# Optimization experiments

Hardware: AMD Instinct MI355X
Metric: run time of the kernel (lower is better)

The kernel has to match this reference:

```python
import jax, jax.numpy as jnp
import numpy as np

L, H, DM, DH, DI = 6, 8, 512, 64, 2048
QLEN, BSZ, MLEN = 256, 32, 256
EPS = 1e-5


def _ln(x, g, b):
    mu = jnp.mean(x, axis=-1, keepdims=True)
    var = jnp.var(x, axis=-1, keepdims=True)
    return (x - mu) * jax.lax.rsqrt(var + EPS) * g + b


def _rel_shift(x):
    # x: [qlen, rlen, bsz, n_head] -> Transformer-XL relative shift
    q, r, b, n = x.shape
    zp = jnp.zeros((q, 1, b, n), x.dtype)
    xp = jnp.concatenate([zp, x], axis=1).reshape(r + 1, q, b, n)
    return xp[1:].reshape(q, r, b, n)


def setup_inputs() -> dict:
    key = jax.random.key(0)
    ks = jax.random.split(key, 12)
    s = 0.02
    return {
        "w": jax.random.normal(ks[0], (QLEN, BSZ, DM), jnp.float32),
        "mems": jax.random.normal(ks[1], (L, MLEN, BSZ, DM), jnp.float32),
        "qkv_w": jax.random.normal(ks[2], (L, DM, 3 * H * DH), jnp.float32) * s,
        "r_net_w": jax.random.normal(ks[3], (L, DM, H * DH), jnp.float32) * s,
        "o_w": jax.random.normal(ks[4], (L, H * DH, DM), jnp.float32) * s,
        "ln1_g": jnp.ones((L, DM), jnp.float32),
        "ln1_b": jnp.zeros((L, DM), jnp.float32),
        "ff_w1": jax.random.normal(ks[5], (L, DM, DI), jnp.float32) * s,
        "ff_b1": jnp.zeros((L, DI), jnp.float32),
        "ff_w2": jax.random.normal(ks[6], (L, DI, DM), jnp.float32) * s,
        "ff_b2": jnp.zeros((L, DM), jnp.float32),
        "ln2_g": jnp.ones((L, DM), jnp.float32),
        "ln2_b": jnp.zeros((L, DM), jnp.float32),
        "r_w_bias": jax.random.normal(ks[7], (H, DH), jnp.float32) * s,
        "r_r_bias": jax.random.normal(ks[8], (H, DH), jnp.float32) * s,
    }


def reference(w, mems, qkv_w, r_net_w, o_w, ln1_g, ln1_b,
              ff_w1, ff_b1, ff_w2, ff_b2, ln2_g, ln2_b,
              r_w_bias, r_r_bias):
    qlen, bsz, d_model = w.shape
    mlen = mems.shape[1]
    klen = qlen + mlen
    scale = 1.0 / (DH ** 0.5)

    # sinusoidal relative positional embedding, pos = klen-1 ... 0
    pos_seq = jnp.arange(klen - 1, -1, -1, dtype=jnp.float32)
    inv_freq = 1.0 / (10000.0 ** (jnp.arange(0, d_model, 2, dtype=jnp.float32) / d_model))
    sinu = pos_seq[:, None] * inv_freq[None, :]
    r = jnp.concatenate([jnp.sin(sinu), jnp.cos(sinu)], axis=-1)  # [klen, d_model]

    # causal mask with memory: query i attends keys j <= i + mlen
    mask = jnp.triu(jnp.ones((qlen, klen), bool), k=1 + mlen)

    h = w
    for l in range(L):
        cat = jnp.concatenate([mems[l], h], axis=0)            # [klen, b, d]
        w_heads = cat @ qkv_w[l]                                # [klen, b, 3HD]
        q, k, v = jnp.split(w_heads, 3, axis=-1)
        q = q[-qlen:].reshape(qlen, bsz, H, DH)
        k = k.reshape(klen, bsz, H, DH)
        v = v.reshape(klen, bsz, H, DH)
        r_head_k = (r @ r_net_w[l]).reshape(klen, H, DH)

        AC = jnp.einsum('ibnd,jbnd->ijbn', q + r_w_bias, k)
        BD = _rel_shift(jnp.einsum('ibnd,jnd->ijbn', q + r_r_bias, r_head_k))
        score = (AC + BD) * scale
        score = jnp.where(mask[:, :, None, None], -jnp.inf, score)
        prob = jax.nn.softmax(score, axis=1)                    # over key dim j
        vec = jnp.einsum('ijbn,jbnd->ibnd', prob, v).reshape(qlen, bsz, H * DH)
        attn_out = vec @ o_w[l]
        h = _ln(h + attn_out, ln1_g[l], ln1_b[l])

        ff = jax.nn.relu(h @ ff_w1[l] + ff_b1[l]) @ ff_w2[l] + ff_b2[l]
        h = _ln(h + ff, ln2_g[l], ln2_b[l])
    return h
```

## Files before the change

kernel.cpp:

```cpp
#include <hip/hip_runtime.h>
#include <math.h>

#define LNUM 6
#define H 8
#define DM 512
#define DH 64
#define DI 2048
#define QLEN 256
#define BSZ 32
#define MLEN 256
#define KLEN (QLEN + MLEN)
#define EPS 1e-5f
#define SCALE 0.125f
#define SN 1024

typedef unsigned short u16;
typedef short bf16x8 __attribute__((ext_vector_type(8)));
typedef short bf16x4 __attribute__((ext_vector_type(4)));
typedef float f32x4 __attribute__((ext_vector_type(4)));

__device__ __forceinline__ u16 f2b(float f) {
    union { float f; unsigned u; } x; x.f = f;
    const unsigned r = x.u + 0x7FFFu + ((x.u >> 16) & 1u);
    return (u16)(r >> 16);
}
__device__ __forceinline__ float b2f(u16 b) {
    union { unsigned u; float f; } x; x.u = (unsigned)b << 16;
    return x.f;
}

__device__ __forceinline__ void gl16(const u16* g, u16* l) {
    __builtin_amdgcn_global_load_lds(
        (const __attribute__((address_space(1))) unsigned int*)g,
        (__attribute__((address_space(3))) unsigned int*)l, 16, 0, 0);
}

template<int TBN, int EPIL>
__global__ __launch_bounds__(256) void mm_bt(
    const u16* __restrict__ A0, const u16* __restrict__ A1, int split,
    const u16* __restrict__ Bt, const u16* __restrict__ Bt2,
    int M, int N, int K,
    long aBatch, long bBatch, int bMask,
    float* __restrict__ Cf, u16* __restrict__ Cb,
    const float* __restrict__ bias,
    u16* __restrict__ o2, u16* __restrict__ o3, u16* __restrict__ o4,
    const float* __restrict__ rwb, const float* __restrict__ rrb,
    int bnBase, int CHp)
{
    constexpr int NT = (TBN == 128) ? 4 : 2;
    __shared__ __align__(16) u16 lds[(128 + TBN) * 32];

    const int tid = threadIdx.x;
    const int w = tid >> 6, lane = tid & 63;
    const int m0 = blockIdx.y * 128;
    const int n0 = blockIdx.x * TBN;

    int z = blockIdx.z;
    int nOff = 0;
    const u16* Ab; const u16* Ab1; const u16* Bb;
    if constexpr (EPIL == 5) {
        const bool rel = (z >= CHp);
        if (rel) { z -= CHp; nOff = 512; }
        Ab = (rel ? A1 : A0) + (size_t)z * aBatch;
        Ab1 = Ab;
        Bb = rel ? (Bt2 + (size_t)(z & 7) * bBatch)
                 : (Bt + (size_t)z * bBatch);
    } else {
        Ab = A0 + (size_t)z * aBatch;
        Ab1 = A1 + (size_t)z * aBatch;
        Bb = Bt + (size_t)(z & bMask) * bBatch;
    }

    const int rt = tid >> 2;
    const int ct = (tid & 3) ^ (rt & 3) ^ ((rt >> 2) & 1);
    const int cofs = ct * 8;

    const int gm1 = m0 + rt, gm2 = m0 + 64 + rt;
    const u16* ap1 = ((gm1 < split) ? Ab + (size_t)gm1 * K
                                    : Ab1 + (size_t)(gm1 - split) * K) + cofs;
    const u16* ap2 = ((gm2 < split) ? Ab + (size_t)gm2 * K
                                    : Ab1 + (size_t)(gm2 - split) * K) + cofs;
    const u16* bp1 = Bb + (size_t)(n0 + rt) * K + cofs;
    const u16* bp2 = (TBN == 128) ? Bb + (size_t)(n0 + 64 + rt) * K + cofs : nullptr;

    u16* ldsA1 = &lds[tid * 8];
    u16* ldsA2 = &lds[2048 + tid * 8];
    u16* ldsB1 = &lds[4096 + tid * 8];
    u16* ldsB2 = &lds[6144 + tid * 8];

    const int wm = (w >> 1) * 64, wn = (w & 1) * (TBN / 2);
    const int fr = lane & 15;
    const int sw = (fr & 3) ^ ((fr >> 2) & 1);
    const int cread = (((lane >> 4) ^ sw) << 4);
    const char* ldsc = (const char*)lds;

    f32x4 acc[4][NT] = {};

    for (int k0 = 0; k0 < K; k0 += 32) {
        __syncthreads();
        gl16(ap1 + k0, ldsA1);
        gl16(ap2 + k0, ldsA2);
        gl16(bp1 + k0, ldsB1);
        if constexpr (TBN == 128) gl16(bp2 + k0, ldsB2);
        __syncthreads();

        bf16x8 af[4], bfr[NT];
#pragma unroll
        for (int mt = 0; mt < 4; mt++)
            af[mt] = *(const bf16x8*)(ldsc + (((wm + mt * 16 + fr) << 6) | cread));
#pragma unroll
        for (int nt = 0; nt < NT; nt++)
            bfr[nt] = *(const bf16x8*)(ldsc + 8192 + (((wn + nt * 16 + fr) << 6) | cread));
#pragma unroll
        for (int mt = 0; mt < 4; mt++)
#pragma unroll
            for (int nt = 0; nt < NT; nt++)
                acc[mt][nt] = __builtin_amdgcn_mfma_f32_16x16x32_bf16(
                    af[mt], bfr[nt], acc[mt][nt], 0, 0, 0);
    }

    const int col = lane & 15, quad = lane >> 4;
#pragma unroll
    for (int mt = 0; mt < 4; mt++)
#pragma unroll
    for (int nt = 0; nt < NT; nt++)
#pragma unroll
    for (int r = 0; r < 4; r++) {
        const int m = m0 + wm + mt * 16 + quad * 4 + r;
        const int n = n0 + wn + nt * 16 + col;
        const float v = acc[mt][nt][r];
        if constexpr (EPIL == 0) {
            Cf[(size_t)m * N + n] = v;
        } else if constexpr (EPIL == 1) {
            Cf[(size_t)m * N + n] = v + bias[n];
        } else if constexpr (EPIL == 2) {
            Cb[(size_t)m * N + n] = f2b(fmaxf(v + bias[n], 0.f));
        } else if constexpr (EPIL == 3) {
            const int kl = m >> 5, b_ = m & 31;
            const int sec = n >> 9, cc = n & 511, hd = cc >> 6, dd = cc & 63;
            const int bh = b_ * H + hd;
            if (sec == 1) o3[((size_t)bh * KLEN + kl) * DH + dd] = f2b(v);
            else if (sec == 2) o4[((size_t)bh * KLEN + kl) * DH + dd] = f2b(v);
            else if (kl >= MLEN) {
                const size_t qi = ((size_t)bh * QLEN + (kl - MLEN)) * DH + dd;
                Cb[qi] = f2b(v + rwb[hd * DH + dd]);
                o2[qi] = f2b(v + rrb[hd * DH + dd]);
            }
        } else if constexpr (EPIL == 4) {
            const int hd = n >> 6, dd = n & 63;
            Cb[(size_t)z * (H * KLEN * DH) +
               ((size_t)hd * KLEN + m) * DH + dd] = f2b(v);
        } else if constexpr (EPIL == 5) {
            Cb[(size_t)z * QLEN * SN + (size_t)m * SN + nOff + n] = f2b(v);
        } else if constexpr (EPIL == 6) {
            const int bn = bnBase + z;
            const int b_ = bn >> 3, nh = bn & 7;
            Cb[((size_t)m * BSZ + b_) * (H * DH) + nh * DH + n] = f2b(v);
        }
    }
}

#define SRELP 100
#define PP 68
__global__ __launch_bounds__(256) void attn_kernel(
    const u16* __restrict__ qw,
    const u16* __restrict__ qrr,
    const u16* __restrict__ kb,
    const u16* __restrict__ vt,
    const u16* __restrict__ rk,
    u16* __restrict__ out)
{
    const int bh = blockIdx.x;
    const int b = bh >> 3, h = bh & 7;
    const int w = threadIdx.x >> 6, lane = threadIdx.x & 63;
    const int fr = lane & 15, ch = lane >> 4;
    const int i0 = blockIdx.y * 128 + w * 32;

    __shared__ __align__(16) u16 lds[4 * (32 * SRELP + 32 * PP)];
    u16* sl = &lds[w * (32 * SRELP + 32 * PP)];
    u16* pl = sl + 32 * SRELP;

    const u16* qwB = qw  + (size_t)bh * QLEN * DH;
    const u16* qrB = qrr + (size_t)bh * QLEN * DH;
    const u16* kbB = kb  + (size_t)bh * KLEN * DH;
    const u16* vtB = vt  + (size_t)bh * DH * KLEN;
    const u16* rkB = rk  + (size_t)h * KLEN * DH;

    bf16x8 qf[2][2], qrf[2][2];
#pragma unroll
    for (int mt = 0; mt < 2; mt++)
#pragma unroll
    for (int kk = 0; kk < 2; kk++) {
        const size_t ro = (size_t)(i0 + mt * 16 + fr) * DH + kk * 32 + ch * 8;
        qf[mt][kk]  = *(const bf16x8*)(qwB + ro);
        qrf[mt][kk] = *(const bf16x8*)(qrB + ro);
    }

    f32x4 o_[2][4] = {};
    float mR[2][4], lR[2][4];
#pragma unroll
    for (int mt = 0; mt < 2; mt++)
#pragma unroll
    for (int r = 0; r < 4; r++) { mR[mt][r] = -1e30f; lR[mt][r] = 0.f; }

    const int T = min(8, ((i0 + 31 + MLEN) >> 6) + 1);
    for (int t = 0; t < T; t++) {
        const int j0 = t * 64;
        const int jr0 = j0 + 224 - i0;

        f32x4 sr[2][6] = {};
#pragma unroll
        for (int kk = 0; kk < 2; kk++) {
            bf16x8 bf_[6];
#pragma unroll
            for (int nt = 0; nt < 6; nt++) {
                int row = jr0 + nt * 16 + fr;
                row = row < KLEN ? row : KLEN - 1;
                bf_[nt] = *(const bf16x8*)(rkB + (size_t)row * DH + kk * 32 + ch * 8);
            }
#pragma unroll
            for (int mt = 0; mt < 2; mt++)
#pragma unroll
            for (int nt = 0; nt < 6; nt++)
                sr[mt][nt] = __builtin_amdgcn_mfma_f32_16x16x32_bf16(
                    qrf[mt][kk], bf_[nt], sr[mt][nt], 0, 0, 0);
        }
#pragma unroll
        for (int mt = 0; mt < 2; mt++)
#pragma unroll
        for (int nt = 0; nt < 6; nt++)
#pragma unroll
        for (int r = 0; r < 4; r++)
            sl[(mt * 16 + ch * 4 + r) * SRELP + nt * 16 + fr] = f2b(sr[mt][nt][r]);

        f32x4 ac[2][4] = {};
#pragma unroll
        for (int kk = 0; kk < 2; kk++) {
            bf16x8 kf[4];
#pragma unroll
            for (int nt = 0; nt < 4; nt++)
                kf[nt] = *(const bf16x8*)(kbB + (size_t)(j0 + nt * 16 + fr) * DH
                                          + kk * 32 + ch * 8);
#pragma unroll
            for (int mt = 0; mt < 2; mt++)
#pragma unroll
            for (int nt = 0; nt < 4; nt++)
                ac[mt][nt] = __builtin_amdgcn_mfma_f32_16x16x32_bf16(
                    qf[mt][kk], kf[nt], ac[mt][nt], 0, 0, 0);
        }

        float s[2][4][4];
#pragma unroll
        for (int mt = 0; mt < 2; mt++)
#pragma unroll
        for (int nt = 0; nt < 4; nt++)
#pragma unroll
        for (int r = 0; r < 4; r++) {
            const int ii = mt * 16 + ch * 4 + r;
            const int jj = nt * 16 + fr;
            float v = (ac[mt][nt][r]
                       + b2f(sl[ii * SRELP + jj + 31 - ii])) * SCALE;
            if (j0 + jj > i0 + ii + MLEN) v = -1e30f;
            s[mt][nt][r] = v;
        }

#pragma unroll
        for (int mt = 0; mt < 2; mt++)
#pragma unroll
        for (int r = 0; r < 4; r++) {
            float tm = fmaxf(fmaxf(s[mt][0][r], s[mt][1][r]),
                             fmaxf(s[mt][2][r], s[mt][3][r]));
#pragma unroll
            for (int d = 1; d < 16; d <<= 1) tm = fmaxf(tm, __shfl_xor(tm, d, 64));
            const float mN = fmaxf(mR[mt][r], tm);
            const float corr = __expf(mR[mt][r] - mN);
            mR[mt][r] = mN;
            float ps = 0.f;
#pragma unroll
            for (int nt = 0; nt < 4; nt++) {
                const float p = __expf(s[mt][nt][r] - mN);
                s[mt][nt][r] = p;
                ps += p;
            }
#pragma unroll
            for (int d = 1; d < 16; d <<= 1) ps += __shfl_xor(ps, d, 64);
            lR[mt][r] = lR[mt][r] * corr + ps;
#pragma unroll
            for (int nt = 0; nt < 4; nt++) o_[mt][nt][r] *= corr;
        }

#pragma unroll
        for (int mt = 0; mt < 2; mt++)
#pragma unroll
        for (int nt = 0; nt < 4; nt++)
#pragma unroll
        for (int r = 0; r < 4; r++)
            pl[(mt * 16 + ch * 4 + r) * PP + nt * 16 + fr] = f2b(s[mt][nt][r]);

        bf16x8 pf[2][2];
#pragma unroll
        for (int mt = 0; mt < 2; mt++)
#pragma unroll
        for (int kk = 0; kk < 2; kk++) {
            const u16* src = pl + (mt * 16 + fr) * PP + kk * 32 + ch * 8;
            union { bf16x8 v; bf16x4 hh[2]; } u;
            u.hh[0] = *(const bf16x4*)src;
            u.hh[1] = *(const bf16x4*)(src + 4);
            pf[mt][kk] = u.v;
        }
#pragma unroll
        for (int kk = 0; kk < 2; kk++) {
            bf16x8 vf[4];
#pragma unroll
            for (int nt = 0; nt < 4; nt++)
                vf[nt] = *(const bf16x8*)(vtB + (size_t)(nt * 16 + fr) * KLEN
                                          + j0 + kk * 32 + ch * 8);
#pragma unroll
            for (int mt = 0; mt < 2; mt++)
#pragma unroll
            for (int nt = 0; nt < 4; nt++)
                o_[mt][nt] = __builtin_amdgcn_mfma_f32_16x16x32_bf16(
                    pf[mt][kk], vf[nt], o_[mt][nt], 0, 0, 0);
        }
    }

#pragma unroll
    for (int mt = 0; mt < 2; mt++)
#pragma unroll
    for (int r = 0; r < 4; r++) {
        const float inv = 1.f / lR[mt][r];
        const int i = i0 + mt * 16 + ch * 4 + r;
#pragma unroll
        for (int nt = 0; nt < 4; nt++) {
            const int d = nt * 16 + fr;
            out[((size_t)i * BSZ + b) * (H * DH) + h * DH + d] =
                f2b(o_[mt][nt][r] * inv);
        }
    }
}

__global__ __launch_bounds__(256) void vtr_kernel(const u16* __restrict__ v,
                                                  u16* __restrict__ vt)
{
    __shared__ u16 t[32][33];
    const int bh = blockIdx.z;
    const int kl0 = blockIdx.x * 32, dd0 = blockIdx.y * 32;
    const int tx = threadIdx.x & 31, ty = threadIdx.x >> 5;
    const u16* src = v + (size_t)bh * KLEN * DH;
#pragma unroll
    for (int r = 0; r < 4; r++)
        t[ty + r * 8][tx] = src[(size_t)(kl0 + ty + r * 8) * DH + dd0 + tx];
    __syncthreads();
    u16* dst = vt + (size_t)bh * DH * KLEN;
#pragma unroll
    for (int r = 0; r < 4; r++)
        dst[(size_t)(dd0 + ty + r * 8) * KLEN + kl0 + tx] = t[tx][ty + r * 8];
}

__global__ __launch_bounds__(256) void tr4_kernel(
    const float* __restrict__ s0, const float* __restrict__ s1,
    const float* __restrict__ s2, const float* __restrict__ s3,
    u16* __restrict__ d0, u16* __restrict__ d1, u16* __restrict__ d2,
    u16* __restrict__ d3)
{
    const float* src; u16* dst; int K, N;
    switch (blockIdx.z) {
        case 0: src = s0; dst = d0; K = 512;  N = 1536; break;
        case 1: src = s1; dst = d1; K = 512;  N = 512;  break;
        case 2: src = s2; dst = d2; K = 512;  N = 2048; break;
        default: src = s3; dst = d3; K = 2048; N = 512; break;
    }
    const int n0 = blockIdx.x * 32, k0 = blockIdx.y * 32;
    if (n0 >= N || k0 >= K) return;
    const int tx = threadIdx.x & 31, ty = threadIdx.x >> 5;
    __shared__ float t[32][33];
#pragma unroll
    for (int r = 0; r < 4; r++)
        t[ty + r * 8][tx] = src[(size_t)(k0 + ty + r * 8) * N + n0 + tx];
    __syncthreads();
#pragma unroll
    for (int r = 0; r < 4; r++)
        dst[(size_t)(n0 + ty + r * 8) * K + k0 + tx] = f2b(t[tx][ty + r * 8]);
}

__global__ __launch_bounds__(256) void trrk_kernel(const float* __restrict__ s,
                                                   u16* __restrict__ d)
{
    const int l = blockIdx.z;
    const float* src = s + (size_t)l * DM * (H * DH);
    u16* dst = d + (size_t)l * DM * (H * DH);
    const int n0 = blockIdx.x * 32, k0 = blockIdx.y * 32;
    const int tx = threadIdx.x & 31, ty = threadIdx.x >> 5;
    __shared__ float t[32][33];
#pragma unroll
    for (int r = 0; r < 4; r++)
        t[ty + r * 8][tx] = src[(size_t)(k0 + ty + r * 8) * (H * DH) + n0 + tx];
    __syncthreads();
#pragma unroll
    for (int r = 0; r < 4; r++)
        dst[(size_t)(n0 + ty + r * 8) * DM + k0 + tx] = f2b(t[tx][ty + r * 8]);
}

__global__ __launch_bounds__(256) void cvt4_kernel(const float* __restrict__ s,
                                                   u16* __restrict__ d)
{
    const int i = blockIdx.x * 256 + threadIdx.x;
    const float4 v = ((const float4*)s)[i];
    ((ushort4*)d)[i] = make_ushort4(f2b(v.x), f2b(v.y), f2b(v.z), f2b(v.w));
}

__global__ __launch_bounds__(256) void copyh_kernel(const float* __restrict__ s,
                                                    float* __restrict__ h,
                                                    u16* __restrict__ hb)
{
    const int i = blockIdx.x * 256 + threadIdx.x;
    const float4 v = ((const float4*)s)[i];
    ((float4*)h)[i] = v;
    ((ushort4*)hb)[i] = make_ushort4(f2b(v.x), f2b(v.y), f2b(v.z), f2b(v.w));
}

__global__ __launch_bounds__(256) void r_kernel(u16* __restrict__ rb)
{
    const int idx = blockIdx.x * 256 + threadIdx.x;
    const int p = idx >> 9, c = idx & 511;
    const float pos = (float)(KLEN - 1 - p);
    const int i2 = (c < 256) ? c : (c - 256);
    const float invf = expf(-((float)(2 * i2) / (float)DM) * logf(10000.0f));
    const float a = pos * invf;
    rb[idx] = f2b((c < 256) ? sinf(a) : cosf(a));
}

__global__ __launch_bounds__(256) void ln_kernel(
    float* __restrict__ h, u16* __restrict__ hb, const float* __restrict__ add,
    const float* __restrict__ g, const float* __restrict__ b)
{
    const int row = blockIdx.x;
    const int t = threadIdx.x;
    const size_t base = (size_t)row * DM;
    const float x0 = h[base + t] + add[base + t];
    const float x1 = h[base + t + 256] + add[base + t + 256];
    float s = x0 + x1;
    float s2 = x0 * x0 + x1 * x1;
#pragma unroll
    for (int off = 32; off > 0; off >>= 1) {
        s += __shfl_down(s, off, 64);
        s2 += __shfl_down(s2, off, 64);
    }
    __shared__ float ws1[4], ws2[4];
    const int wid = t >> 6, lane = t & 63;
    if (lane == 0) { ws1[wid] = s; ws2[wid] = s2; }
    __syncthreads();
    __shared__ float mv[2];
    if (t == 0) {
        float a = 0.f, a2 = 0.f;
        for (int wv = 0; wv < 4; wv++) { a += ws1[wv]; a2 += ws2[wv]; }
        const float mean = a / (float)DM;
        mv[0] = mean;
        mv[1] = rsqrtf(a2 / (float)DM - mean * mean + EPS);
    }
    __syncthreads();
    const float mean = mv[0], rstd = mv[1];
    const float r0 = (x0 - mean) * rstd * g[t] + b[t];
    const float r1 = (x1 - mean) * rstd * g[t + 256] + b[t + 256];
    h[base + t] = r0;
    h[base + t + 256] = r1;
    hb[base + t] = f2b(r0);
    hb[base + t + 256] = f2b(r1);
}

extern "C" void kernel_launch(void* const* d_in, const int* in_sizes, int n_in,
                              void* d_out, int out_size, void* d_ws, size_t ws_size,
                              hipStream_t stream)
{
    const float* w      = (const float*)d_in[0];
    const float* mems   = (const float*)d_in[1];
    const float* qkv_w  = (const float*)d_in[2];
    const float* rnet_w = (const float*)d_in[3];
    const float* o_w    = (const float*)d_in[4];
    const float* ln1_g  = (const float*)d_in[5];
    const float* ln1_b  = (const float*)d_in[6];
    const float* ff_w1  = (const float*)d_in[7];
    const float* ff_b1  = (const float*)d_in[8];
    const float* ff_w2  = (const float*)d_in[9];
    const float* ff_b2  = (const float*)d_in[10];
    const float* ln2_g  = (const float*)d_in[11];
    const float* ln2_b  = (const float*)d_in[12];
    const float* rwb    = (const float*)d_in[13];
    const float* rrb    = (const float*)d_in[14];

    char* p = (char*)d_ws;
    auto alloc = [&](size_t bytes) { void* r = p; p += (bytes + 255) & ~(size_t)255; return r; };

    const int HD = H * DH;

    float* hbuf  = (float*)alloc((size_t)QLEN * BSZ * DM * 4);
    u16*   hb    = (u16*)alloc((size_t)QLEN * BSZ * DM * 2);
    u16*   rb    = (u16*)alloc((size_t)KLEN * DM * 2);
    u16*   memsb = (u16*)alloc((size_t)MLEN * BSZ * DM * 2);
    u16*   qkvwt = (u16*)alloc((size_t)DM * 3 * HD * 2);
    u16*   owt   = (u16*)alloc((size_t)HD * DM * 2);
    u16*   f1wt  = (u16*)alloc((size_t)DM * DI * 2);
    u16*   f2wt  = (u16*)alloc((size_t)DI * DM * 2);
    u16*   rkwtA = (u16*)alloc((size_t)LNUM * DM * HD * 2);
    u16*   rkbA  = (u16*)alloc((size_t)LNUM * H * KLEN * DH * 2);
    u16*   vecb  = (u16*)alloc((size_t)QLEN * BSZ * DM * 2);
    u16*   vtb   = (u16*)alloc((size_t)BSZ * H * DH * KLEN * 2);
    char*  R1    = (char*)alloc((size_t)QLEN * BSZ * DM * 4);
    char*  R2    = (char*)alloc((size_t)QLEN * BSZ * DI * 2);
    u16*   qwb = (u16*)R1;
    u16*   qrb = (u16*)(R1 + (size_t)BSZ * H * QLEN * DH * 2);
    float* atmp = (float*)R1;
    float* ff2t = (float*)R1;
    u16*   kb  = (u16*)R2;
    u16*   vb  = (u16*)(R2 + (size_t)BSZ * H * KLEN * DH * 2);
    u16*   ff1b = (u16*)R2;

    const int BIG = 1 << 30;

    copyh_kernel<<<(QLEN * BSZ * DM) / 1024, 256, 0, stream>>>(w, hbuf, hb);
    r_kernel<<<(KLEN * DM) / 256, 256, 0, stream>>>(rb);
    trrk_kernel<<<dim3(16, 16, LNUM), 256, 0, stream>>>(rnet_w, rkwtA);
    mm_bt<128, 4><<<dim3(4, 4, LNUM), 256, 0, stream>>>(
        rb, rb, BIG, rkwtA, nullptr,
        KLEN, HD, DM, 0, (long)DM * HD, 7,
        nullptr, rkbA, nullptr, nullptr, nullptr, nullptr, nullptr, nullptr, 0, 0);

    for (int l = 0; l < LNUM; l++) {
        cvt4_kernel<<<(MLEN * BSZ * DM) / 1024, 256, 0, stream>>>(
            mems + (size_t)l * MLEN * BSZ * DM, memsb);
        tr4_kernel<<<dim3(64, 64, 4), 256, 0, stream>>>(
            qkv_w + (size_t)l * DM * 3 * HD, o_w + (size_t)l * HD * DM,
            ff_w1 + (size_t)l * DM * DI, ff_w2 + (size_t)l * DI * DM,
            qkvwt, owt, f1wt, f2wt);

        mm_bt<128, 3><<<dim3(12, 128, 1), 256, 0, stream>>>(
            memsb, hb, MLEN * BSZ, qkvwt, nullptr,
            KLEN * BSZ, 3 * HD, DM, 0, 0, 0,
            nullptr, qwb, nullptr, qrb, kb, vb, rwb, rrb, 0, 0);
        vtr_kernel<<<dim3(16, 2, BSZ * H), 256, 0, stream>>>(vb, vtb);

        attn_kernel<<<dim3(BSZ * H, 2), 256, 0, stream>>>(
            qwb, qrb, kb, vtb, rkbA + (size_t)l * H * KLEN * DH, vecb);

        mm_bt<128, 0><<<dim3(4, 64, 1), 256, 0, stream>>>(
            vecb, vecb, BIG, owt, nullptr,
            QLEN * BSZ, DM, HD, 0, 0, 0,
            atmp, nullptr, nullptr, nullptr, nullptr, nullptr, nullptr, nullptr, 0, 0);
        ln_kernel<<<QLEN * BSZ, 256, 0, stream>>>(hbuf, hb, atmp,
                                                  ln1_g + l * DM, ln1_b + l * DM);
        mm_bt<128, 2><<<dim3(16, 64, 1), 256, 0, stream>>>(
            hb, hb, BIG, f1wt, nullptr,
            QLEN * BSZ, DI, DM, 0, 0, 0,
            nullptr, ff1b, ff_b1 + (size_t)l * DI, nullptr, nullptr, nullptr,
            nullptr, nullptr, 0, 0);
        mm_bt<128, 1><<<dim3(4, 64, 1), 256, 0, stream>>>(
            ff1b, ff1b, BIG, f2wt, nullptr,
            QLEN * BSZ, DM, DI, 0, 0, 0,
            ff2t, nullptr, ff_b2 + (size_t)l * DM, nullptr, nullptr, nullptr,
            nullptr, nullptr, 0, 0);
        ln_kernel<<<QLEN * BSZ, 256, 0, stream>>>(hbuf, hb, ff2t,
                                                  ln2_g + l * DM, ln2_b + l * DM);
    }
    hipMemcpyAsync(d_out, hbuf, (size_t)out_size * sizeof(float),
                   hipMemcpyDeviceToDevice, stream);
}
```

Measured before the change: 1.754 ms.

## Shrink attention tiles to 16 rows per wave, remap GEMM blocks by XCD, fold scale into Q

```diff
diff --git a/kernel.cpp b/kernel.cpp
--- a/kernel.cpp
+++ b/kernel.cpp
@@ -52,8 +52,17 @@
 
     const int tid = threadIdx.x;
     const int w = tid >> 6, lane = tid & 63;
-    const int m0 = blockIdx.y * 128;
-    const int n0 = blockIdx.x * TBN;
+
+    const int nwgx = gridDim.x;
+    const int nwg = nwgx * gridDim.y;
+    int flat = blockIdx.x + nwgx * blockIdx.y;
+    {
+        const int q = nwg >> 3, r8 = nwg & 7;
+        const int xcd = flat & 7, loc = flat >> 3;
+        flat = (xcd < r8 ? xcd * (q + 1) : r8 * (q + 1) + (xcd - r8) * q) + loc;
+    }
+    const int m0 = (flat / nwgx) * 128;
+    const int n0 = (flat % nwgx) * TBN;
 
     int z = blockIdx.z;
     int nOff = 0;
@@ -143,8 +152,8 @@
             else if (sec == 2) o4[((size_t)bh * KLEN + kl) * DH + dd] = f2b(v);
             else if (kl >= MLEN) {
                 const size_t qi = ((size_t)bh * QLEN + (kl - MLEN)) * DH + dd;
-                Cb[qi] = f2b(v + rwb[hd * DH + dd]);
-                o2[qi] = f2b(v + rrb[hd * DH + dd]);
+                Cb[qi] = f2b((v + rwb[hd * DH + dd]) * SCALE);
+                o2[qi] = f2b((v + rrb[hd * DH + dd]) * SCALE);
             }
         } else if constexpr (EPIL == 4) {
             const int hd = n >> 6, dd = n & 63;
@@ -160,9 +169,9 @@
     }
 }
 
-#define SRELP 100
+#define SRELP 84
 #define PP 68
-__global__ __launch_bounds__(256) void attn_kernel(
+__global__ __launch_bounds__(256, 4) void attn_kernel(
     const u16* __restrict__ qw,
     const u16* __restrict__ qrr,
     const u16* __restrict__ kb,
@@ -174,11 +183,11 @@
     const int b = bh >> 3, h = bh & 7;
     const int w = threadIdx.x >> 6, lane = threadIdx.x & 63;
     const int fr = lane & 15, ch = lane >> 4;
-    const int i0 = blockIdx.y * 128 + w * 32;
-
-    __shared__ __align__(16) u16 lds[4 * (32 * SRELP + 32 * PP)];
-    u16* sl = &lds[w * (32 * SRELP + 32 * PP)];
-    u16* pl = sl + 32 * SRELP;
+    const int i0 = blockIdx.y * 64 + w * 16;
+
+    __shared__ __align__(16) u16 lds[4 * (16 * SRELP + 16 * PP)];
+    u16* sl = &lds[w * (16 * SRELP + 16 * PP)];
+    u16* pl = sl + 16 * SRELP;
 
     const u16* qwB = qw  + (size_t)bh * QLEN * DH;
     const u16* qrB = qrr + (size_t)bh * QLEN * DH;
@@ -186,54 +195,46 @@
     const u16* vtB = vt  + (size_t)bh * DH * KLEN;
     const u16* rkB = rk  + (size_t)h * KLEN * DH;
 
-    bf16x8 qf[2][2], qrf[2][2];
-#pragma unroll
-    for (int mt = 0; mt < 2; mt++)
+    bf16x8 qf[2], qrf[2];
 #pragma unroll
     for (int kk = 0; kk < 2; kk++) {
-        const size_t ro = (size_t)(i0 + mt * 16 + fr) * DH + kk * 32 + ch * 8;
-        qf[mt][kk]  = *(const bf16x8*)(qwB + ro);
-        qrf[mt][kk] = *(const bf16x8*)(qrB + ro);
-    }
-
-    f32x4 o_[2][4] = {};
-    float mR[2][4], lR[2][4];
-#pragma unroll
-    for (int mt = 0; mt < 2; mt++)
-#pragma unroll
-    for (int r = 0; r < 4; r++) { mR[mt][r] = -1e30f; lR[mt][r] = 0.f; }
-
-    const int T = min(8, ((i0 + 31 + MLEN) >> 6) + 1);
+        const size_t ro = (size_t)(i0 + fr) * DH + kk * 32 + ch * 8;
+        qf[kk]  = *(const bf16x8*)(qwB + ro);
+        qrf[kk] = *(const bf16x8*)(qrB + ro);
+    }
+
+    f32x4 o_[4] = {};
+    float mR[4], lR[4];
+#pragma unroll
+    for (int r = 0; r < 4; r++) { mR[r] = -1e30f; lR[r] = 0.f; }
+
+    const int T = ((i0 + 15 + MLEN) >> 6) + 1;
     for (int t = 0; t < T; t++) {
         const int j0 = t * 64;
-        const int jr0 = j0 + 224 - i0;
-
-        f32x4 sr[2][6] = {};
+        const int jr0 = j0 + 240 - i0;
+
+        f32x4 sr[5] = {};
 #pragma unroll
         for (int kk = 0; kk < 2; kk++) {
-            bf16x8 bf_[6];
-#pragma unroll
-            for (int nt = 0; nt < 6; nt++) {
+            bf16x8 bf_[5];
+#pragma unroll
+            for (int nt = 0; nt < 5; nt++) {
                 int row = jr0 + nt * 16 + fr;
                 row = row < KLEN ? row : KLEN - 1;
                 bf_[nt] = *(const bf16x8*)(rkB + (size_t)row * DH + kk * 32 + ch * 8);
             }
 #pragma unroll
-            for (int mt = 0; mt < 2; mt++)
-#pragma unroll
-            for (int nt = 0; nt < 6; nt++)
-                sr[mt][nt] = __builtin_amdgcn_mfma_f32_16x16x32_bf16(
-                    qrf[mt][kk], bf_[nt], sr[mt][nt], 0, 0, 0);
-        }
-#pragma unroll
-        for (int mt = 0; mt < 2; mt++)
-#pragma unroll
-        for (int nt = 0; nt < 6; nt++)
+            for (int nt = 0; nt < 5; nt++)
+                sr[nt] = __builtin_amdgcn_mfma_f32_16x16x32_bf16(
+                    qrf[kk], bf_[nt], sr[nt], 0, 0, 0);
+        }
+#pragma unroll
+        for (int nt = 0; nt < 5; nt++)
 #pragma unroll
         for (int r = 0; r < 4; r++)
-            sl[(mt * 16 + ch * 4 + r) * SRELP + nt * 16 + fr] = f2b(sr[mt][nt][r]);
-
-        f32x4 ac[2][4] = {};
+            sl[(ch * 4 + r) * SRELP + nt * 16 + fr] = f2b(sr[nt][r]);
+
+        f32x4 ac[4] = {};
 #pragma unroll
         for (int kk = 0; kk < 2; kk++) {
             bf16x8 kf[4];
@@ -242,71 +243,65 @@
                 kf[nt] = *(const bf16x8*)(kbB + (size_t)(j0 + nt * 16 + fr) * DH
                                           + kk * 32 + ch * 8);
 #pragma unroll
-            for (int mt = 0; mt < 2; mt++)
-#pragma unroll
             for (int nt = 0; nt < 4; nt++)
-                ac[mt][nt] = __builtin_amdgcn_mfma_f32_16x16x32_bf16(
-                    qf[mt][kk], kf[nt], ac[mt][nt], 0, 0, 0);
-        }
-
-        float s[2][4][4];
-#pragma unroll
-        for (int mt = 0; mt < 2; mt++)
+                ac[nt] = __builtin_amdgcn_mfma_f32_16x16x32_bf16(
+                    qf[kk], kf[nt], ac[nt], 0, 0, 0);
+        }
+
+        float s[4][4];
 #pragma unroll
         for (int nt = 0; nt < 4; nt++)
 #pragma unroll
         for (int r = 0; r < 4; r++) {
-            const int ii = mt * 16 + ch * 4 + r;
+            const int ii = ch * 4 + r;
             const int jj = nt * 16 + fr;
-            float v = (ac[mt][nt][r]
-                       + b2f(sl[ii * SRELP + jj + 31 - ii])) * SCALE;
-            if (j0 + jj > i0 + ii + MLEN) v = -1e30f;
-            s[mt][nt][r] = v;
-        }
-
-#pragma unroll
-        for (int mt = 0; mt < 2; mt++)
+            s[nt][r] = ac[nt][r] + b2f(sl[ii * SRELP + jj + 15 - ii]);
+        }
+        if (t == T - 1) {
+#pragma unroll
+            for (int nt = 0; nt < 4; nt++)
+#pragma unroll
+            for (int r = 0; r < 4; r++)
+                if (j0 + nt * 16 + fr > i0 + ch * 4 + r + MLEN)
+                    s[nt][r] = -1e30f;
+        }
+
 #pragma unroll
         for (int r = 0; r < 4; r++) {
-            float tm = fmaxf(fmaxf(s[mt][0][r], s[mt][1][r]),
-                             fmaxf(s[mt][2][r], s[mt][3][r]));
+            float tm = fmaxf(fmaxf(s[0][r], s[1][r]), fmaxf(s[2][r], s[3][r]));
 #pragma unroll
             for (int d = 1; d < 16; d <<= 1) tm = fmaxf(tm, __shfl_xor(tm, d, 64));
-            const float mN = fmaxf(mR[mt][r], tm);
-            const float corr = __expf(mR[mt][r] - mN);
-            mR[mt][r] = mN;
+            const float mN = fmaxf(mR[r], tm);
+            const float corr = __expf(mR[r] - mN);
+            mR[r] = mN;
             float ps = 0.f;
 #pragma unroll
             for (int nt = 0; nt < 4; nt++) {
-                const float p = __expf(s[mt][nt][r] - mN);
-                s[mt][nt][r] = p;
+                const float p = __expf(s[nt][r] - mN);
+                s[nt][r] = p;
                 ps += p;
             }
 #pragma unroll
             for (int d = 1; d < 16; d <<= 1) ps += __shfl_xor(ps, d, 64);
-            lR[mt][r] = lR[mt][r] * corr + ps;
-#pragma unroll
-            for (int nt = 0; nt < 4; nt++) o_[mt][nt][r] *= corr;
-        }
-
-#pragma unroll
-        for (int mt = 0; mt < 2; mt++)
+            lR[r] = lR[r] * corr + ps;
+#pragma unroll
+            for (int nt = 0; nt < 4; nt++) o_[nt][r] *= corr;
+        }
+
 #pragma unroll
         for (int nt = 0; nt < 4; nt++)
 #pragma unroll
         for (int r = 0; r < 4; r++)
-            pl[(mt * 16 + ch * 4 + r) * PP + nt * 16 + fr] = f2b(s[mt][nt][r]);
-
-        bf16x8 pf[2][2];
-#pragma unroll
-        for (int mt = 0; mt < 2; mt++)
+            pl[(ch * 4 + r) * PP + nt * 16 + fr] = f2b(s[nt][r]);
+
+        bf16x8 pf[2];
 #pragma unroll
         for (int kk = 0; kk < 2; kk++) {
-            const u16* src = pl + (mt * 16 + fr) * PP + kk * 32 + ch * 8;
+            const u16* src = pl + fr * PP + kk * 32 + ch * 8;
             union { bf16x8 v; bf16x4 hh[2]; } u;
             u.hh[0] = *(const bf16x4*)src;
             u.hh[1] = *(const bf16x4*)(src + 4);
-            pf[mt][kk] = u.v;
+            pf[kk] = u.v;
         }
 #pragma unroll
         for (int kk = 0; kk < 2; kk++) {
@@ -316,25 +311,21 @@
                 vf[nt] = *(const bf16x8*)(vtB + (size_t)(nt * 16 + fr) * KLEN
                                           + j0 + kk * 32 + ch * 8);
 #pragma unroll
-            for (int mt = 0; mt < 2; mt++)
-#pragma unroll
             for (int nt = 0; nt < 4; nt++)
-                o_[mt][nt] = __builtin_amdgcn_mfma_f32_16x16x32_bf16(
-                    pf[mt][kk], vf[nt], o_[mt][nt], 0, 0, 0);
-        }
-    }
-
-#pragma unroll
-    for (int mt = 0; mt < 2; mt++)
+                o_[nt] = __builtin_amdgcn_mfma_f32_16x16x32_bf16(
+                    pf[kk], vf[nt], o_[nt], 0, 0, 0);
+        }
+    }
+
 #pragma unroll
     for (int r = 0; r < 4; r++) {
-        const float inv = 1.f / lR[mt][r];
-        const int i = i0 + mt * 16 + ch * 4 + r;
+        const float inv = 1.f / lR[r];
+        const int i = i0 + ch * 4 + r;
 #pragma unroll
         for (int nt = 0; nt < 4; nt++) {
             const int d = nt * 16 + fr;
             out[((size_t)i * BSZ + b) * (H * DH) + h * DH + d] =
-                f2b(o_[mt][nt][r] * inv);
+                f2b(o_[nt][r] * inv);
         }
     }
 }
@@ -539,7 +530,7 @@
             nullptr, qwb, nullptr, qrb, kb, vb, rwb, rrb, 0, 0);
         vtr_kernel<<<dim3(16, 2, BSZ * H), 256, 0, stream>>>(vb, vtb);
 
-        attn_kernel<<<dim3(BSZ * H, 2), 256, 0, stream>>>(
+        attn_kernel<<<dim3(BSZ * H, 4), 256, 0, stream>>>(
             qwb, qrb, kb, vtb, rkbA + (size_t)l * H * KLEN * DH, vecb);
 
         mm_bt<128, 0><<<dim3(4, 64, 1), 256, 0, stream>>>(
```

Result: slower. 1.881 ms (+7.2%).
